# Kernel optimization log

Hardware: AMD Instinct MI355X
Metric: run time of the kernel (lower is better)

## Reference

```python
import jax, jax.numpy as jnp
import numpy as np

B, Hg, Wg, DIM, HEADS, WS, SHIFT = 16, 64, 64, 512, 16, 8, 4
HIDDEN = 4 * DIM
PRIOR_BETA = 1.0
EPS = 1e-5


def _layernorm(x, g, b):
    m = jnp.mean(x, axis=-1, keepdims=True)
    v = jnp.mean(jnp.square(x - m), axis=-1, keepdims=True)
    return (x - m) / jnp.sqrt(v + EPS) * g + b


def _rel_pos_index(ws):
    coords = np.stack(np.meshgrid(np.arange(ws), np.arange(ws), indexing='ij')).reshape(2, -1)
    rel = (coords[:, :, None] - coords[:, None, :]).transpose(1, 2, 0)
    rel[..., 0] += ws - 1
    rel[..., 1] += ws - 1
    rel[..., 0] *= 2 * ws - 1
    return rel.sum(-1)  # (N, N) int


def _shift_mask(H, W, ws, shift):
    img = np.zeros((H, W))
    cnt = 0
    for hs in (slice(0, -ws), slice(-ws, -shift), slice(-shift, None)):
        for wsl in (slice(0, -ws), slice(-ws, -shift), slice(-shift, None)):
            img[hs, wsl] = cnt
            cnt += 1
    N = ws * ws
    mw = img.reshape(H // ws, ws, W // ws, ws).transpose(0, 2, 1, 3).reshape(-1, N)
    am = mw[:, None, :] - mw[:, :, None]
    return np.where(am != 0, -100.0, 0.0).astype(np.float32)  # (nW, N, N)


def setup_inputs() -> dict:
    key = jax.random.key(0)
    ks = jax.random.split(key, 8)
    s = 0.02
    return {
        'x': jax.random.normal(ks[0], (B, Hg * Wg, DIM), jnp.float32),
        'M_map': jax.random.uniform(ks[1], (B, Hg, Wg, 1), jnp.float32),
        'norm1_g': jnp.ones((DIM,), jnp.float32),
        'norm1_b': jnp.zeros((DIM,), jnp.float32),
        'qkv_w': jax.random.normal(ks[2], (3 * DIM, DIM), jnp.float32) * s,
        'qkv_b': jnp.zeros((3 * DIM,), jnp.float32),
        'proj_w': jax.random.normal(ks[3], (DIM, DIM), jnp.float32) * s,
        'proj_b': jnp.zeros((DIM,), jnp.float32),
        'rpb_table': jax.random.normal(ks[4], ((2 * WS - 1) ** 2, HEADS), jnp.float32) * s,
        'norm2_g': jnp.ones((DIM,), jnp.float32),
        'norm2_b': jnp.zeros((DIM,), jnp.float32),
        'fc1_w': jax.random.normal(ks[5], (HIDDEN, DIM), jnp.float32) * s,
        'fc1_b': jnp.zeros((HIDDEN,), jnp.float32),
        'fc2_w': jax.random.normal(ks[6], (DIM, HIDDEN), jnp.float32) * s,
        'fc2_b': jnp.zeros((DIM,), jnp.float32),
        'H': Hg,
        'W': Wg,
    }


def reference(x, M_map, norm1_g, norm1_b, qkv_w, qkv_b, proj_w, proj_b, rpb_table,
              norm2_g, norm2_b, fc1_w, fc1_b, fc2_w, fc2_b, H, W):
    Bsz, L, C = x.shape
    ws, shift, heads = WS, SHIFT, HEADS
    N = ws * ws
    hd = C // heads
    scale = hd ** -0.5

    shortcut = x
    y = _layernorm(x, norm1_g, norm1_b).reshape(Bsz, H, W, C)
    Mm = jnp.clip(M_map[..., 0], 0.0, 1.0)  # (B, H, W)

    # cyclic shift (SW-MSA)
    y = jnp.roll(y, (-shift, -shift), axis=(1, 2))
    Mm = jnp.roll(Mm, (-shift, -shift), axis=(1, 2))

    # window partition -> (B*nW, N, C) and (B*nW, N)
    def win_part(t):
        c = t.shape[-1]
        t = t.reshape(Bsz, H // ws, ws, W // ws, ws, c)
        return t.transpose(0, 1, 3, 2, 4, 5).reshape(-1, N, c)

    xw = win_part(y)
    mw = win_part(Mm[..., None])[..., 0]
    B_ = xw.shape[0]

    qkv = (xw @ qkv_w.T + qkv_b).reshape(B_, N, 3, heads, hd).transpose(2, 0, 3, 1, 4)
    q, k, v = qkv[0], qkv[1], qkv[2]  # each (B_, heads, N, hd)
    attn = jnp.einsum('bhnd,bhmd->bhnm', q * scale, k)

    # relative position bias (heads, N, N)
    rpi = _rel_pos_index(ws)
    rpb = rpb_table[rpi.reshape(-1)].reshape(N, N, heads).transpose(2, 0, 1)
    attn = attn + rpb[None]

    # semantic prior bias: 0.5*(M_i + M_j), broadcast over heads
    sb = 0.5 * (mw[:, :, None] + mw[:, None, :])  # (B_, N, N)
    attn = attn + PRIOR_BETA * sb[:, None]

    # shift mask
    am = jnp.asarray(_shift_mask(H, W, ws, shift), attn.dtype)  # (nW, N, N)
    nW = am.shape[0]
    attn = attn.reshape(Bsz, nW, heads, N, N) + am[None, :, None]
    attn = attn.reshape(B_, heads, N, N)

    attn = jax.nn.softmax(attn, axis=-1)
    out = jnp.einsum('bhnm,bhmd->bhnd', attn, v).transpose(0, 2, 1, 3).reshape(B_, N, C)
    out = out @ proj_w.T + proj_b

    # window reverse + reverse shift
    out = out.reshape(Bsz, H // ws, W // ws, ws, ws, C).transpose(0, 1, 3, 2, 4, 5).reshape(Bsz, H, W, C)
    out = jnp.roll(out, (shift, shift), axis=(1, 2)).reshape(Bsz, L, C)

    x1 = shortcut + out
    h = jax.nn.gelu(_layernorm(x1, norm2_g, norm2_b) @ fc1_w.T + fc1_b, approximate=False)
    return x1 + (h @ fc2_w.T + fc2_b)
```

## Files before the change

### kernel.cpp

```cpp
#include <hip/hip_runtime.h>
#include <hip/hip_bf16.h>

typedef unsigned short u16;
typedef unsigned int u32;
typedef __attribute__((ext_vector_type(4))) float f32x4;
typedef __attribute__((ext_vector_type(8))) short bf16x8;

#define DEV static __device__ __forceinline__

DEV float bf2f(u16 u) { u32 x = ((u32)u) << 16; return __builtin_bit_cast(float, x); }
DEV u16 f2bf(float f) {
  __hip_bfloat16 h = __float2bfloat16(f);
  return __builtin_bit_cast(u16, h);
}

DEV void gld16(const u16* g, u16* l) {
  __builtin_amdgcn_global_load_lds((const __attribute__((address_space(1))) void*)g,
                                   (__attribute__((address_space(3))) void*)l, 16, 0, 0);
}

__global__ void cvt_bf16(const float* __restrict__ s, u16* __restrict__ d, int n) {
  int i = blockIdx.x * 256 + threadIdx.x;
  if (i < n) d[i] = f2bf(s[i]);
}

__global__ __launch_bounds__(256)
void ln_bf16(const float* __restrict__ src, const float* __restrict__ g,
             const float* __restrict__ b, u16* __restrict__ dst) {
  const int row = blockIdx.x * 4 + (threadIdx.x >> 6);
  const int lane = threadIdx.x & 63;
  const float* p = src + (long)row * 512 + lane * 8;
  float x[8];
  *(float4*)&x[0] = *(const float4*)p;
  *(float4*)&x[4] = *(const float4*)(p + 4);
  float s = 0.f;
#pragma unroll
  for (int e = 0; e < 8; ++e) s += x[e];
#pragma unroll
  for (int off = 32; off; off >>= 1) s += __shfl_xor(s, off, 64);
  const float mean = s * (1.0f / 512.0f);
  float q = 0.f;
#pragma unroll
  for (int e = 0; e < 8; ++e) { float d = x[e] - mean; q += d * d; }
#pragma unroll
  for (int off = 32; off; off >>= 1) q += __shfl_xor(q, off, 64);
  const float rinv = rsqrtf(q * (1.0f / 512.0f) + 1e-5f);
  u16 o[8];
  const int c0 = lane * 8;
#pragma unroll
  for (int e = 0; e < 8; ++e) o[e] = f2bf((x[e] - mean) * rinv * g[c0 + e] + b[c0 + e]);
  *(uint4*)(dst + (long)row * 512 + c0) = *(uint4*)o;
}

constexpr int BM = 128, BN = 128, BK = 32;

enum { EPI_QKV = 0, EPI_PROJ = 1, EPI_GELU = 2, EPI_FC2 = 3 };

template <int EPI>
__global__ __launch_bounds__(256)
void gemm_nt(const u16* __restrict__ A, const u16* __restrict__ W,
             const float* __restrict__ bias, const float* __restrict__ res,
             void* __restrict__ outv, int M, int N, int K) {
  __shared__ u16 As[BM * BK];
  __shared__ u16 Bs[BN * BK];
  const int t = threadIdx.x;
  const int lane = t & 63;
  const int wave = t >> 6;
  const int wm = (wave >> 1) * 64;
  const int wn = (wave & 1) * 64;
  const long m0 = (long)blockIdx.y * BM;
  const long n0 = (long)blockIdx.x * BN;

  const int r0 = wave * 16 + (lane >> 2);
  const int kel = (lane & 3) * 8;
  const u16* gA0 = A + (m0 + r0) * (long)K + kel;
  const u16* gA1 = gA0 + 64L * K;
  const u16* gB0 = W + (n0 + r0) * (long)K + kel;
  const u16* gB1 = gB0 + 64L * K;
  u16* lA0 = As + wave * 512;
  u16* lA1 = As + (4 + wave) * 512;
  u16* lB0 = Bs + wave * 512;
  u16* lB1 = Bs + (4 + wave) * 512;

  f32x4 acc[4][4] = {};
  const int fr = lane & 15, koff = (lane >> 4) * 8;

  for (int k0 = 0; k0 < K; k0 += BK) {
    gld16(gA0 + k0, lA0);
    gld16(gA1 + k0, lA1);
    gld16(gB0 + k0, lB0);
    gld16(gB1 + k0, lB1);
    __syncthreads();
    bf16x8 af[4], bff[4];
#pragma unroll
    for (int i = 0; i < 4; ++i) af[i] = *(const bf16x8*)&As[(wm + i * 16 + fr) * BK + koff];
#pragma unroll
    for (int j = 0; j < 4; ++j) bff[j] = *(const bf16x8*)&Bs[(wn + j * 16 + fr) * BK + koff];
#pragma unroll
    for (int i = 0; i < 4; ++i)
#pragma unroll
      for (int j = 0; j < 4; ++j)
        acc[i][j] = __builtin_amdgcn_mfma_f32_16x16x32_bf16(af[i], bff[j], acc[i][j], 0, 0, 0);
    __syncthreads();
  }

  const int col = lane & 15;
  const int rq = (lane >> 4) * 4;
#pragma unroll
  for (int i = 0; i < 4; ++i) {
#pragma unroll
    for (int j = 0; j < 4; ++j) {
#pragma unroll
      for (int r = 0; r < 4; ++r) {
        const long m = m0 + wm + i * 16 + rq + r;
        const long n = n0 + wn + j * 16 + col;
        const float v = acc[i][j][r] + bias[n];
        const long idx = m * (long)N + n;
        if constexpr (EPI == EPI_QKV) {
          ((u16*)outv)[idx] = f2bf(v);
        } else if constexpr (EPI == EPI_PROJ) {
          ((float*)outv)[idx] = v + res[idx];
        } else if constexpr (EPI == EPI_GELU) {
          ((u16*)outv)[idx] = f2bf(0.5f * v * (1.0f + erff(v * 0.70710678118f)));
        } else {
          ((float*)outv)[idx] = v + res[idx];
        }
      }
    }
  }
}

constexpr int SS_S = 68;
constexpr int VT_S = 72;

__global__ __launch_bounds__(256)
void attn_mfma(const u16* __restrict__ qkv, const float* __restrict__ mmap,
               const float* __restrict__ rpb, u16* __restrict__ outp) {
  __shared__ u16 SSb[4 * 64 * SS_S];
  __shared__ u16 Vtb[4 * 32 * VT_S];
  __shared__ u16 rpb_s[16 * 226];
  __shared__ float mw[64];
  __shared__ int tok[64];
  __shared__ int regi[64];

  const int t = threadIdx.x;
  const int lane = t & 63, wave = t >> 6;
  const int c = lane & 15, q = lane >> 4;
  const int win = blockIdx.x;
  const int b = win >> 6, wh = (win >> 3) & 7, ww = win & 7;

  if (t < 64) {
    const int i = t >> 3, j = t & 7;
    const int hs = wh * 8 + i, wsv = ww * 8 + j;
    const int h = (hs + 4) & 63, w = (wsv + 4) & 63;
    const int tk = b * 4096 + h * 64 + w;
    tok[t] = tk;
    mw[t] = fminf(fmaxf(mmap[tk], 0.f), 1.f);
    regi[t] = (hs < 56 ? 0 : (hs < 60 ? 1 : 2)) * 3 + (wsv < 56 ? 0 : (wsv < 60 ? 1 : 2));
  }
  for (int id = t; id < 3600; id += 256) {
    const int h = id & 15, idx = id >> 4;
    rpb_s[h * 226 + idx] = f2bf(rpb[id]);
  }
  __syncthreads();

  u16* SS = SSb + wave * 64 * SS_S;
  u16* Vt = Vtb + wave * 32 * VT_S;

  int tQ[4];
  float mwn[16], mwm[4];
  int rgn[16], rgm[4];
#pragma unroll
  for (int i = 0; i < 4; ++i) tQ[i] = tok[16 * i + c];
#pragma unroll
  for (int i = 0; i < 4; ++i)
#pragma unroll
    for (int r = 0; r < 4; ++r) {
      const int n = 16 * i + 4 * q + r;
      mwn[i * 4 + r] = mw[n];
      rgn[i * 4 + r] = regi[n];
    }
#pragma unroll
  for (int j = 0; j < 4; ++j) {
    const int m = 16 * j + c;
    mwm[j] = mw[m];
    rgm[j] = regi[m];
  }
  const int imc = c >> 3, jmc = c & 7;
  const int tV = tok[lane];
  const float scale = 0.17677669529663687f;

  for (int hi = 0; hi < 4; ++hi) {
    const int head = wave * 4 + hi;

    bf16x8 qf[4], kf[4];
#pragma unroll
    for (int i = 0; i < 4; ++i) {
      const u16* base = qkv + (long)tQ[i] * 1536 + head * 32 + q * 8;
      qf[i] = *(const bf16x8*)(base);
      kf[i] = *(const bf16x8*)(base + 512);
    }

    {
      const u16* vp = qkv + (long)tV * 1536 + 1024 + head * 32;
      u16 vv[32];
      *(uint4*)&vv[0]  = *(const uint4*)(vp);
      *(uint4*)&vv[8]  = *(const uint4*)(vp + 8);
      *(uint4*)&vv[16] = *(const uint4*)(vp + 16);
      *(uint4*)&vv[24] = *(const uint4*)(vp + 24);
#pragma unroll
      for (int d = 0; d < 32; ++d) Vt[d * VT_S + lane] = vv[d];
    }

    f32x4 acc[4][4] = {};
#pragma unroll
    for (int i = 0; i < 4; ++i)
#pragma unroll
      for (int j = 0; j < 4; ++j)
        acc[i][j] = __builtin_amdgcn_mfma_f32_16x16x32_bf16(qf[i], kf[j], acc[i][j], 0, 0, 0);

    const u16* rb = rpb_s + head * 226;
    float rmx[16], rsum[16];
#pragma unroll
    for (int i = 0; i < 4; ++i)
#pragma unroll
      for (int r = 0; r < 4; ++r) {
        const int n = 16 * i + 4 * q + r;
        const int inr = n >> 3, jnr = n & 7;
        float mx = -1e30f;
#pragma unroll
        for (int j = 0; j < 4; ++j) {
          const int di = inr - 2 * j - imc + 7;
          const int dj = jnr - jmc + 7;
          float s = acc[i][j][r] * scale + bf2f(rb[di * 15 + dj]) +
                    0.5f * (mwn[i * 4 + r] + mwm[j]);
          if (rgn[i * 4 + r] != rgm[j]) s -= 100.f;
          acc[i][j][r] = s;
          mx = fmaxf(mx, s);
        }
        rmx[i * 4 + r] = mx;
      }
#pragma unroll
    for (int ir = 0; ir < 16; ++ir)
#pragma unroll
      for (int msk = 1; msk < 16; msk <<= 1)
        rmx[ir] = fmaxf(rmx[ir], __shfl_xor(rmx[ir], msk, 64));
#pragma unroll
    for (int i = 0; i < 4; ++i)
#pragma unroll
      for (int r = 0; r < 4; ++r) {
        float sm = 0.f;
#pragma unroll
        for (int j = 0; j < 4; ++j) {
          const float e = __expf(acc[i][j][r] - rmx[i * 4 + r]);
          acc[i][j][r] = e;
          sm += e;
        }
        rsum[i * 4 + r] = sm;
      }
#pragma unroll
    for (int ir = 0; ir < 16; ++ir) {
#pragma unroll
      for (int msk = 1; msk < 16; msk <<= 1)
        rsum[ir] += __shfl_xor(rsum[ir], msk, 64);
      rsum[ir] = 1.0f / rsum[ir];
    }

#pragma unroll
    for (int i = 0; i < 4; ++i)
#pragma unroll
      for (int j = 0; j < 4; ++j) {
        ushort4 pk;
        pk.x = f2bf(acc[i][j][0] * rsum[i * 4 + 0]);
        pk.y = f2bf(acc[i][j][1] * rsum[i * 4 + 1]);
        pk.z = f2bf(acc[i][j][2] * rsum[i * 4 + 2]);
        pk.w = f2bf(acc[i][j][3] * rsum[i * 4 + 3]);
        *(ushort4*)&SS[(16 * j + c) * SS_S + 16 * i + 4 * q] = pk;
      }

    __syncthreads();

    bf16x8 av[2][2];
#pragma unroll
    for (int mi = 0; mi < 2; ++mi)
#pragma unroll
      for (int ki = 0; ki < 2; ++ki)
        av[mi][ki] = *(const bf16x8*)&Vt[(16 * mi + c) * VT_S + 32 * ki + 8 * q];

    f32x4 oacc[2][4] = {};
#pragma unroll
    for (int ki = 0; ki < 2; ++ki)
#pragma unroll
      for (int ni = 0; ni < 4; ++ni) {
        union { u16 h[8]; bf16x8 v; } ub;
#pragma unroll
        for (int jj = 0; jj < 8; ++jj)
          ub.h[jj] = SS[(32 * ki + 8 * q + jj) * SS_S + 16 * ni + c];
#pragma unroll
        for (int mi = 0; mi < 2; ++mi)
          oacc[mi][ni] = __builtin_amdgcn_mfma_f32_16x16x32_bf16(av[mi][ki], ub.v, oacc[mi][ni], 0, 0, 0);
      }

#pragma unroll
    for (int ni = 0; ni < 4; ++ni) {
      u16* ob = outp + (long)tQ[ni] * 512 + head * 32;
#pragma unroll
      for (int mi = 0; mi < 2; ++mi) {
        ushort4 pk;
        pk.x = f2bf(oacc[mi][ni][0]);
        pk.y = f2bf(oacc[mi][ni][1]);
        pk.z = f2bf(oacc[mi][ni][2]);
        pk.w = f2bf(oacc[mi][ni][3]);
        *(ushort4*)(ob + 16 * mi + 4 * q) = pk;
      }
    }
    __syncthreads();
  }
}

extern "C" void kernel_launch(void* const* d_in, const int* in_sizes, int n_in,
                              void* d_out, int out_size, void* d_ws, size_t ws_size,
                              hipStream_t stream) {
  (void)in_sizes; (void)n_in; (void)out_size; (void)ws_size;
  const float* x      = (const float*)d_in[0];
  const float* mmap   = (const float*)d_in[1];
  const float* n1g    = (const float*)d_in[2];
  const float* n1b    = (const float*)d_in[3];
  const float* qkv_w  = (const float*)d_in[4];
  const float* qkv_b  = (const float*)d_in[5];
  const float* proj_w = (const float*)d_in[6];
  const float* proj_b = (const float*)d_in[7];
  const float* rpb    = (const float*)d_in[8];
  const float* n2g    = (const float*)d_in[9];
  const float* n2b    = (const float*)d_in[10];
  const float* fc1_w  = (const float*)d_in[11];
  const float* fc1_b  = (const float*)d_in[12];
  const float* fc2_w  = (const float*)d_in[13];
  const float* fc2_b  = (const float*)d_in[14];
  float* out = (float*)d_out;
  char* ws = (char*)d_ws;

  u16*   ybf   = (u16*)(ws);
  u16*   qkvbf = (u16*)(ws + (64L  << 20));
  u16*   attno = (u16*)(ws + (256L << 20));
  float* x1    = (float*)(ws + (320L << 20));
  u16*   hbuf  = qkvbf;
  u16*   wqkv  = (u16*)(ws + (448L << 20));
  u16*   wproj = wqkv + 1536 * 512;
  u16*   wfc1  = wproj + 512 * 512;
  u16*   wfc2  = wfc1 + 2048 * 512;

  cvt_bf16<<<1536 * 512 / 256, 256, 0, stream>>>(qkv_w, wqkv, 1536 * 512);
  cvt_bf16<<<512 * 512 / 256, 256, 0, stream>>>(proj_w, wproj, 512 * 512);
  cvt_bf16<<<2048 * 512 / 256, 256, 0, stream>>>(fc1_w, wfc1, 2048 * 512);
  cvt_bf16<<<512 * 2048 / 256, 256, 0, stream>>>(fc2_w, wfc2, 512 * 2048);

  ln_bf16<<<16384, 256, 0, stream>>>(x, n1g, n1b, ybf);
  gemm_nt<EPI_QKV><<<dim3(12, 512), 256, 0, stream>>>(ybf, wqkv, qkv_b, nullptr, qkvbf, 65536, 1536, 512);
  attn_mfma<<<1024, 256, 0, stream>>>(qkvbf, mmap, rpb, attno);
  gemm_nt<EPI_PROJ><<<dim3(4, 512), 256, 0, stream>>>(attno, wproj, proj_b, x, x1, 65536, 512, 512);
  ln_bf16<<<16384, 256, 0, stream>>>(x1, n2g, n2b, ybf);
  gemm_nt<EPI_GELU><<<dim3(16, 512), 256, 0, stream>>>(ybf, wfc1, fc1_b, nullptr, hbuf, 65536, 2048, 512);
  gemm_nt<EPI_FC2><<<dim3(4, 512), 256, 0, stream>>>(hbuf, wfc2, fc2_b, x1, out, 65536, 512, 2048);
}
```

Baseline: 1.204 ms.

## Replace GEMM with 256x256 tiles and a four-stage LDS pipeline

Replaces the 128x128 single-buffered GEMM with 256x256 tiles computed by 512 threads. Each wave owns a 128x64 sub-tile. A four-slot ring of direct global-to-LDS loads uses explicit vmcnt waits, so loads run up to three tiles ahead of compute, and MFMA sections get raised wave priority. The aim is more data reuse per tile and less barrier stall. In exchange it uses 128KB of dynamic LDS per block, larger accumulator register pressure, and fewer blocks (e.g. 512 for the proj/fc2 GEMMs).

```diff
diff --git a/kernel.cpp b/kernel.cpp
--- a/kernel.cpp
+++ b/kernel.cpp
@@ -52,69 +52,103 @@
   *(uint4*)(dst + (long)row * 512 + c0) = *(uint4*)o;
 }
 
-constexpr int BM = 128, BN = 128, BK = 32;
-
 enum { EPI_QKV = 0, EPI_PROJ = 1, EPI_GELU = 2, EPI_FC2 = 3 };
 
 template <int EPI>
-__global__ __launch_bounds__(256)
-void gemm_nt(const u16* __restrict__ A, const u16* __restrict__ W,
+__global__ __launch_bounds__(512, 2)
+void gemm256(const u16* __restrict__ A, const u16* __restrict__ W,
              const float* __restrict__ bias, const float* __restrict__ res,
              void* __restrict__ outv, int M, int N, int K) {
-  __shared__ u16 As[BM * BK];
-  __shared__ u16 Bs[BN * BK];
+  extern __shared__ u16 sm[];
+  (void)M;
   const int t = threadIdx.x;
   const int lane = t & 63;
   const int wave = t >> 6;
-  const int wm = (wave >> 1) * 64;
-  const int wn = (wave & 1) * 64;
-  const long m0 = (long)blockIdx.y * BM;
-  const long n0 = (long)blockIdx.x * BN;
-
-  const int r0 = wave * 16 + (lane >> 2);
-  const int kel = (lane & 3) * 8;
-  const u16* gA0 = A + (m0 + r0) * (long)K + kel;
-  const u16* gA1 = gA0 + 64L * K;
-  const u16* gB0 = W + (n0 + r0) * (long)K + kel;
-  const u16* gB1 = gB0 + 64L * K;
-  u16* lA0 = As + wave * 512;
-  u16* lA1 = As + (4 + wave) * 512;
-  u16* lB0 = Bs + wave * 512;
-  u16* lB1 = Bs + (4 + wave) * 512;
-
-  f32x4 acc[4][4] = {};
+  const int wm = wave >> 2;
+  const int wn = wave & 3;
+  const long m0 = (long)blockIdx.y * 256;
+  const long n0 = (long)blockIdx.x * 256;
+
+  const int sr = t >> 2;
+  const int sc = (t & 3) * 8;
+  const u16* gA0 = A + (m0 + sr) * (long)K + sc;
+  const u16* gA1 = gA0 + 128L * K;
+  const u16* gB0 = W + (n0 + sr) * (long)K + sc;
+  const u16* gB1 = gB0 + 128L * K;
+  u16* lws = sm + wave * 512;
+
+  const int NT = K >> 5;
+  f32x4 acc[8][4] = {};
   const int fr = lane & 15, koff = (lane >> 4) * 8;
 
-  for (int k0 = 0; k0 < K; k0 += BK) {
-    gld16(gA0 + k0, lA0);
-    gld16(gA1 + k0, lA1);
-    gld16(gB0 + k0, lB0);
-    gld16(gB1 + k0, lB1);
-    __syncthreads();
-    bf16x8 af[4], bff[4];
-#pragma unroll
-    for (int i = 0; i < 4; ++i) af[i] = *(const bf16x8*)&As[(wm + i * 16 + fr) * BK + koff];
-#pragma unroll
-    for (int j = 0; j < 4; ++j) bff[j] = *(const bf16x8*)&Bs[(wn + j * 16 + fr) * BK + koff];
-#pragma unroll
-    for (int i = 0; i < 4; ++i)
-#pragma unroll
-      for (int j = 0; j < 4; ++j)
-        acc[i][j] = __builtin_amdgcn_mfma_f32_16x16x32_bf16(af[i], bff[j], acc[i][j], 0, 0, 0);
-    __syncthreads();
-  }
+#define STAGE(slot, tile)                      \
+  do {                                         \
+    const int _k = (tile) * 32;                \
+    u16* _b = lws + (slot) * 16384;            \
+    gld16(gA0 + _k, _b);                       \
+    gld16(gA1 + _k, _b + 4096);                \
+    gld16(gB0 + _k, _b + 8192);                \
+    gld16(gB1 + _k, _b + 12288);               \
+  } while (0)
+
+#define COMPUTE(slot)                                                                           \
+  do {                                                                                          \
+    const u16* Ab = sm + (slot) * 16384 + (wm * 128 + fr) * 32 + koff;                          \
+    const u16* Bb = sm + (slot) * 16384 + 8192 + (wn * 64 + fr) * 32 + koff;                    \
+    bf16x8 af[8], bfv[4];                                                                       \
+    _Pragma("unroll")                                                                           \
+    for (int i = 0; i < 8; ++i) af[i] = *(const bf16x8*)(Ab + i * 512);                         \
+    _Pragma("unroll")                                                                           \
+    for (int j = 0; j < 4; ++j) bfv[j] = *(const bf16x8*)(Bb + j * 512);                        \
+    __builtin_amdgcn_s_setprio(1);                                                              \
+    _Pragma("unroll")                                                                           \
+    for (int i = 0; i < 8; ++i)                                                                 \
+      _Pragma("unroll")                                                                         \
+      for (int j = 0; j < 4; ++j)                                                               \
+        acc[i][j] = __builtin_amdgcn_mfma_f32_16x16x32_bf16(af[i], bfv[j], acc[i][j], 0, 0, 0); \
+    __builtin_amdgcn_s_setprio(0);                                                              \
+  } while (0)
+
+  STAGE(0, 0);
+  STAGE(1, 1);
+  STAGE(2, 2);
+  asm volatile("s_waitcnt vmcnt(8)" ::: "memory");
+  __builtin_amdgcn_s_barrier();
+  asm volatile("" ::: "memory");
+
+  int kt = 0;
+  for (; kt < NT - 3; ++kt) {
+    STAGE((kt + 3) & 3, kt + 3);
+    COMPUTE(kt & 3);
+    asm volatile("s_waitcnt vmcnt(8)" ::: "memory");
+    __builtin_amdgcn_s_barrier();
+    asm volatile("" ::: "memory");
+  }
+  COMPUTE(kt & 3);
+  asm volatile("s_waitcnt vmcnt(4)" ::: "memory");
+  __builtin_amdgcn_s_barrier();
+  asm volatile("" ::: "memory");
+  ++kt;
+  COMPUTE(kt & 3);
+  asm volatile("s_waitcnt vmcnt(0)" ::: "memory");
+  __builtin_amdgcn_s_barrier();
+  asm volatile("" ::: "memory");
+  ++kt;
+  COMPUTE(kt & 3);
+#undef STAGE
+#undef COMPUTE
 
   const int col = lane & 15;
   const int rq = (lane >> 4) * 4;
 #pragma unroll
-  for (int i = 0; i < 4; ++i) {
-#pragma unroll
-    for (int j = 0; j < 4; ++j) {
+  for (int mi = 0; mi < 8; ++mi) {
+#pragma unroll
+    for (int ni = 0; ni < 4; ++ni) {
 #pragma unroll
       for (int r = 0; r < 4; ++r) {
-        const long m = m0 + wm + i * 16 + rq + r;
-        const long n = n0 + wn + j * 16 + col;
-        const float v = acc[i][j][r] + bias[n];
+        const long m = m0 + wm * 128 + mi * 16 + rq + r;
+        const long n = n0 + wn * 64 + ni * 16 + col;
+        const float v = acc[mi][ni][r] + bias[n];
         const long idx = m * (long)N + n;
         if constexpr (EPI == EPI_QKV) {
           ((u16*)outv)[idx] = f2bf(v);
@@ -350,16 +384,29 @@
   u16*   wfc1  = wproj + 512 * 512;
   u16*   wfc2  = wfc1 + 2048 * 512;
 
+  static bool smem_init = false;
+  if (!smem_init) {
+    smem_init = true;
+    (void)hipFuncSetAttribute(reinterpret_cast<const void*>(gemm256<EPI_QKV>),
+                              hipFuncAttributeMaxDynamicSharedMemorySize, 131072);
+    (void)hipFuncSetAttribute(reinterpret_cast<const void*>(gemm256<EPI_PROJ>),
+                              hipFuncAttributeMaxDynamicSharedMemorySize, 131072);
+    (void)hipFuncSetAttribute(reinterpret_cast<const void*>(gemm256<EPI_GELU>),
+                              hipFuncAttributeMaxDynamicSharedMemorySize, 131072);
+    (void)hipFuncSetAttribute(reinterpret_cast<const void*>(gemm256<EPI_FC2>),
+                              hipFuncAttributeMaxDynamicSharedMemorySize, 131072);
+  }
+
   cvt_bf16<<<1536 * 512 / 256, 256, 0, stream>>>(qkv_w, wqkv, 1536 * 512);
   cvt_bf16<<<512 * 512 / 256, 256, 0, stream>>>(proj_w, wproj, 512 * 512);
   cvt_bf16<<<2048 * 512 / 256, 256, 0, stream>>>(fc1_w, wfc1, 2048 * 512);
   cvt_bf16<<<512 * 2048 / 256, 256, 0, stream>>>(fc2_w, wfc2, 512 * 2048);
 
   ln_bf16<<<16384, 256, 0, stream>>>(x, n1g, n1b, ybf);
-  gemm_nt<EPI_QKV><<<dim3(12, 512), 256, 0, stream>>>(ybf, wqkv, qkv_b, nullptr, qkvbf, 65536, 1536, 512);
+  gemm256<EPI_QKV><<<dim3(6, 256), 512, 131072, stream>>>(ybf, wqkv, qkv_b, nullptr, qkvbf, 65536, 1536, 512);
   attn_mfma<<<1024, 256, 0, stream>>>(qkvbf, mmap, rpb, attno);
-  gemm_nt<EPI_PROJ><<<dim3(4, 512), 256, 0, stream>>>(attno, wproj, proj_b, x, x1, 65536, 512, 512);
+  gemm256<EPI_PROJ><<<dim3(2, 256), 512, 131072, stream>>>(attno, wproj, proj_b, x, x1, 65536, 512, 512);
   ln_bf16<<<16384, 256, 0, stream>>>(x1, n2g, n2b, ybf);
-  gemm_nt<EPI_GELU><<<dim3(16, 512), 256, 0, stream>>>(ybf, wfc1, fc1_b, nullptr, hbuf, 65536, 2048, 512);
-  gemm_nt<EPI_FC2><<<dim3(4, 512), 256, 0, stream>>>(hbuf, wfc2, fc2_b, x1, out, 65536, 512, 2048);
-}
+  gemm256<EPI_GELU><<<dim3(8, 256), 512, 131072, stream>>>(ybf, wfc1, fc1_b, nullptr, hbuf, 65536, 2048, 512);
+  gemm256<EPI_FC2><<<dim3(2, 256), 512, 131072, stream>>>(hbuf, wfc2, fc2_b, x1, out, 65536, 512, 2048);
+}
```

New measurement: 1.185 ms. About the same (-1.6%).
